# Performance work log

Hardware: AMD Instinct MI355X
Metric: run time of the kernel (lower is better)

The kernel has to match this reference:

```python
import jax, jax.numpy as jnp
import numpy as np

ALPHA = 0.5
SIGMA = 0.1
EPS = 1e-7
N, T = 8192, 512


def setup_inputs() -> dict:
    key = jax.random.key(0)
    k1, k2, k3 = jax.random.split(key, 3)
    logits = jax.random.normal(k1, (N, T), dtype=jnp.float32)
    pmf = jax.nn.softmax(logits, axis=-1)  # valid PMF rows
    times = jax.random.uniform(k2, (N,), dtype=jnp.float32, minval=0.0, maxval=float(T))
    events = jax.random.randint(k3, (N,), 0, 2).astype(jnp.int32)
    time_bins = jnp.arange(T, dtype=jnp.float32)
    return {"pmf": pmf, "times": times, "events": events, "time_bins": time_bins}


def reference(pmf, times, events, time_bins):
    n, t = pmf.shape
    # torch.bucketize(right=False) == searchsorted side='left'
    bin_idx = jnp.clip(jnp.searchsorted(time_bins, times, side='left') - 1, 0, t - 1)

    cdf = jnp.cumsum(pmf, axis=1)                 # (N, T)
    rows = jnp.arange(n)
    pmf_at = pmf[rows, bin_idx]                   # pmf[i, bin_idx[i]]
    cdf_at = cdf[rows, bin_idx]                   # cdf[i, bin_idx[i]]
    total = cdf[:, -1]
    surv = total - cdf_at + pmf_at                # sum pmf[i, bin_idx[i]:]

    nll = jnp.where(events == 1, -jnp.log(pmf_at + EPS), -jnp.log(surv + EPS))
    loss = nll.mean()

    # Pairwise ranking term (vectorized over event anchors i and later samples j)
    later = times[None, :] > times[:, None]       # later[i, j] = times[j] > times[i]
    cnt = later.sum(axis=1)                       # (N,) number of later samples per i
    G = cdf[:, bin_idx].T                         # G[i, j] = cdf[j, bin_idx[i]]
    e = jnp.exp((G - cdf_at[:, None]) / SIGMA)    # exp(diff / sigma)
    per_i = jnp.sum(jnp.where(later, e, 0.0), axis=1) / jnp.maximum(cnt, 1)
    valid = (events == 1) & (cnt > 0)
    n_pairs = valid.sum()
    rank_loss = jnp.sum(jnp.where(valid, per_i, 0.0))

    apply_rank = (events.sum() > 1) & (n_pairs > 0) & (ALPHA > 0)
    loss = jnp.where(apply_rank, loss + ALPHA * rank_loss / jnp.maximum(n_pairs, 1), loss)
    return loss
```

## Files before the change

kernel.cpp:

```cpp
#include <hip/hip_runtime.h>
#include <cstdint>
#include <cstddef>

#define SIGMA_INV 10.0f
#define EPS_C 1e-7f

constexpr int TDIM = 512;
constexpr int ROWS2 = 16;
constexpr int PITCH = 513;
constexpr int NBLK = 512;
constexpr int MAXC = 256;
constexpr int GSTRIDE = 32;

__device__ __forceinline__ void stf(float* p, float v) {
    __hip_atomic_store(p, v, __ATOMIC_RELAXED, __HIP_MEMORY_SCOPE_AGENT);
}
__device__ __forceinline__ void sti(int* p, int v) {
    __hip_atomic_store(p, v, __ATOMIC_RELAXED, __HIP_MEMORY_SCOPE_AGENT);
}
__device__ __forceinline__ float ldf(const float* p) {
    return __hip_atomic_load(p, __ATOMIC_RELAXED, __HIP_MEMORY_SCOPE_AGENT);
}
__device__ __forceinline__ int ldi(const int* p) {
    return __hip_atomic_load(p, __ATOMIC_RELAXED, __HIP_MEMORY_SCOPE_AGENT);
}

__global__ __launch_bounds__(512, 4) void rows_kernel(
    const float* __restrict__ pmf, const float* __restrict__ times,
    const int* __restrict__ events, const float* __restrict__ bins,
    unsigned* __restrict__ tkt,
    float* __restrict__ SGTp, float* __restrict__ scaleA,
    float* __restrict__ einvA, int* __restrict__ kidxA,
    float* __restrict__ nll_part, int* __restrict__ ev_part, int N)
{
    __shared__ float tile[ROWS2 * PITCH];
    __shared__ float binsS[TDIM];
    __shared__ int karr[ROWS2];
    __shared__ float nllv[ROWS2];
    __shared__ int evv[ROWS2];
    const int tid = threadIdx.x;
    const int lane = tid & 63;
    const int wid = tid >> 6;
    const int b = blockIdx.x;
    const int i0 = b * ROWS2;

    if (b == 0) {
        for (int w = tid; w < 65 * GSTRIDE; w += 512) tkt[w] = 0u;
    }

    binsS[tid] = bins[tid];

    float4 A[2][2];
    #pragma unroll
    for (int r = 0; r < 2; ++r) {
        const int i = i0 + wid * 2 + r;
        const float4* p4 = (const float4*)(pmf + (size_t)i * TDIM + lane * 8);
        A[r][0] = p4[0];
        A[r][1] = p4[1];
    }
    #pragma unroll
    for (int r = 0; r < 2; ++r) {
        const int rl = wid * 2 + r;
        float c0 = A[r][0].x, c1 = c0 + A[r][0].y, c2 = c1 + A[r][0].z, c3 = c2 + A[r][0].w;
        float c4 = c3 + A[r][1].x, c5 = c4 + A[r][1].y, c6 = c5 + A[r][1].z, c7 = c6 + A[r][1].w;
        float v = c7;
        #pragma unroll
        for (int d = 1; d < 64; d <<= 1) {
            float u = __shfl_up(v, d);
            if (lane >= d) v += u;
        }
        const float excl = v - c7;
        float* t = tile + rl * PITCH + lane * 8;
        t[0] = c0 + excl; t[1] = c1 + excl; t[2] = c2 + excl; t[3] = c3 + excl;
        t[4] = c4 + excl; t[5] = c5 + excl; t[6] = c6 + excl; t[7] = c7 + excl;
    }
    __syncthreads();

    if (tid < ROWS2) {
        const int i = i0 + tid;
        const float t = times[i];
        int lo = 0, hi = TDIM;
        while (lo < hi) {
            int mid = (lo + hi) >> 1;
            if (binsS[mid] < t) lo = mid + 1; else hi = mid;
        }
        int k = lo - 1;
        k = k < 0 ? 0 : (k > TDIM - 1 ? TDIM - 1 : k);
        const float cdf_at = tile[tid * PITCH + k];
        const float tot = tile[tid * PITCH + (TDIM - 1)];
        const float pmf_at = pmf[(size_t)i * TDIM + k];
        const float surv = tot - cdf_at + pmf_at;
        nllv[tid] = (events[i] == 1) ? -logf(pmf_at + EPS_C) : -logf(surv + EPS_C);
        evv[tid] = events[i];
        scaleA[i] = expf(-cdf_at * SIGMA_INV);
        einvA[i] = expf(cdf_at * SIGMA_INV);
        kidxA[i] = k;
        karr[tid] = k;
    }
    __syncthreads();

    float acc = 0.f;
    #pragma unroll
    for (int s = 0; s < ROWS2; ++s) {
        const float c = tile[s * PITCH + tid];
        if (tid < karr[s]) acc += expf(c * SIGMA_INV);
    }
    SGTp[(size_t)b * TDIM + tid] = acc;

    if (wid == 0) {
        float nv = (lane < ROWS2) ? nllv[lane] : 0.f;
        int ev = (lane < ROWS2) ? evv[lane] : 0;
        #pragma unroll
        for (int d = 8; d > 0; d >>= 1) {
            nv += __shfl_down(nv, d);
            ev += __shfl_down(ev, d);
        }
        if (lane == 0) { nll_part[b] = nv; ev_part[b] = ev; }
    }
}

__global__ __launch_bounds__(512, 4) void bucket_final_kernel(
    const float* __restrict__ SGTp, const float* __restrict__ times,
    const int* __restrict__ events, const int* __restrict__ kidxA,
    const float* __restrict__ scaleA, const float* __restrict__ einvA,
    const float* __restrict__ nll_part, const int* __restrict__ ev_part,
    unsigned* __restrict__ tkt,
    float* __restrict__ rank_part, int* __restrict__ npair_part,
    float* __restrict__ out, int N)
{
    __shared__ float redf[8];
    __shared__ int redi[8];
    __shared__ float red2f[8];
    __shared__ int red2i[8];
    __shared__ int cj[MAXC], oj[MAXC];
    __shared__ float mt[MAXC], me[MAXC];
    __shared__ int ncl_sh;
    __shared__ float SGT_sh;
    __shared__ int CGT_sh;
    __shared__ int last_sh;
    __shared__ double sd1[NBLK];
    __shared__ double sd2[NBLK];
    __shared__ int si1[NBLK];
    __shared__ int si2[NBLK];

    const int k = blockIdx.x;
    const int tid = threadIdx.x;
    const int lane = tid & 63;
    const int wid = tid >> 6;

    if (tid == 0) ncl_sh = 0;
    __syncthreads();

    float sv = SGTp[(size_t)tid * TDIM + k];
    #pragma unroll
    for (int d = 32; d > 0; d >>= 1) sv += __shfl_down(sv, d);
    if (lane == 0) redf[wid] = sv;

    int cnt = 0;
    const int4* kx4 = (const int4*)kidxA;
    #pragma unroll
    for (int it = 0; it < 4; ++it) {
        const int ch = it * 512 + tid;
        const int4 kx = kx4[ch];
        const int j0 = ch * 4;
        cnt += (kx.x > k) + (kx.y > k) + (kx.z > k) + (kx.w > k);
        if (kx.x == k) { int p = atomicAdd(&ncl_sh, 1); if (p < MAXC) cj[p] = j0 + 0; }
        if (kx.y == k) { int p = atomicAdd(&ncl_sh, 1); if (p < MAXC) cj[p] = j0 + 1; }
        if (kx.z == k) { int p = atomicAdd(&ncl_sh, 1); if (p < MAXC) cj[p] = j0 + 2; }
        if (kx.w == k) { int p = atomicAdd(&ncl_sh, 1); if (p < MAXC) cj[p] = j0 + 3; }
    }
    #pragma unroll
    for (int d = 32; d > 0; d >>= 1) cnt += __shfl_down(cnt, d);
    if (lane == 0) redi[wid] = cnt;
    __syncthreads();
    if (tid == 0) {
        float s8 = 0.f; int c8 = 0;
        #pragma unroll
        for (int w = 0; w < 8; ++w) { s8 += redf[w]; c8 += redi[w]; }
        SGT_sh = s8; CGT_sh = c8;
    }
    __syncthreads();

    const int nc = ncl_sh < MAXC ? ncl_sh : MAXC;
    if (tid < nc) {
        const int myj = cj[tid];
        int r = 0;
        for (int m = 0; m < nc; ++m) r += (cj[m] < myj) ? 1 : 0;
        oj[r] = myj;
    }
    __syncthreads();
    if (tid < nc) { mt[tid] = times[oj[tid]]; me[tid] = einvA[oj[tid]]; }
    __syncthreads();

    float pi = 0.f;
    int vf = 0;
    if (tid < nc) {
        const int i = oj[tid];
        const float ti = mt[tid];
        float s = 0.f;
        int c = 0;
        for (int m = 0; m < nc; ++m) {
            if (mt[m] > ti) { s += me[m]; c++; }
        }
        const int C = CGT_sh + c;
        if (events[i] == 1 && C > 0) {
            vf = 1;
            pi = scaleA[i] * (SGT_sh + s) / (float)C;
        }
    }
    #pragma unroll
    for (int d = 32; d > 0; d >>= 1) {
        pi += __shfl_down(pi, d);
        vf += __shfl_down(vf, d);
    }
    if (lane == 0) { red2f[wid] = pi; red2i[wid] = vf; }
    __syncthreads();
    if (tid == 0) {
        float s8 = 0.f; int c8 = 0;
        #pragma unroll
        for (int w = 0; w < 8; ++w) { s8 += red2f[w]; c8 += red2i[w]; }
        stf(rank_part + k, s8);
        sti(npair_part + k, c8);
    }

    __syncthreads();
    if (tid == 0) {
        asm volatile("s_waitcnt vmcnt(0)" ::: "memory");
        int is_last = 0;
        unsigned g = __hip_atomic_fetch_add(tkt + (k & 63) * GSTRIDE, 1u,
                                            __ATOMIC_RELAXED,
                                            __HIP_MEMORY_SCOPE_AGENT);
        if (g == 7u) {
            unsigned l2 = __hip_atomic_fetch_add(tkt + 64 * GSTRIDE, 1u,
                                                 __ATOMIC_RELAXED,
                                                 __HIP_MEMORY_SCOPE_AGENT);
            if (l2 == 63u) is_last = 1;
        }
        last_sh = is_last;
    }
    __syncthreads();
    if (!last_sh) return;

    sd1[tid] = (double)nll_part[tid];
    si2[tid] = ev_part[tid];
    sd2[tid] = (double)ldf(rank_part + tid);
    si1[tid] = ldi(npair_part + tid);
    __syncthreads();
    for (int off = 256; off > 0; off >>= 1) {
        if (tid < off) {
            sd1[tid] += sd1[tid + off];
            sd2[tid] += sd2[tid + off];
            si1[tid] += si1[tid + off];
            si2[tid] += si2[tid + off];
        }
        __syncthreads();
    }
    if (tid == 0) {
        double loss = sd1[0] / (double)N;
        if (si2[0] > 1 && si1[0] > 0) loss += 0.5 * sd2[0] / (double)si1[0];
        out[0] = (float)loss;
    }
}

extern "C" void kernel_launch(void* const* d_in, const int* in_sizes, int n_in,
                              void* d_out, int out_size, void* d_ws, size_t ws_size,
                              hipStream_t stream) {
    const float* pmf = (const float*)d_in[0];
    const float* times = (const float*)d_in[1];
    const int* events = (const int*)d_in[2];
    const float* bins = (const float*)d_in[3];
    const int N = in_sizes[1];

    char* ws = (char*)d_ws;
    unsigned* tkt = (unsigned*)ws;
    float* SGTp = (float*)(ws + 16384);
    float* scaleA = SGTp + (size_t)NBLK * TDIM;
    float* einvA = scaleA + N;
    float* nll_part = einvA + N;
    float* rank_part = nll_part + NBLK;
    int* kidxA = (int*)(rank_part + TDIM);
    int* ev_part = kidxA + N;
    int* npair_part = ev_part + NBLK;

    rows_kernel<<<NBLK, 512, 0, stream>>>(
        pmf, times, events, bins, tkt, SGTp, scaleA, einvA, kidxA,
        nll_part, ev_part, N);
    bucket_final_kernel<<<NBLK, 512, 0, stream>>>(
        SGTp, times, events, kidxA, scaleA, einvA, nll_part, ev_part,
        tkt, rank_part, npair_part, (float*)d_out, N);
}
```

Baseline: 23.93 us.

## Build per-bin histogram and member lists in rows kernel instead of rescanning indices

After: 31.18 us. 1.3x slower.

```diff
diff --git a/kernel.cpp b/kernel.cpp
--- a/kernel.cpp
+++ b/kernel.cpp
@@ -6,9 +6,10 @@
 #define EPS_C 1e-7f
 
 constexpr int TDIM = 512;
-constexpr int ROWS2 = 16;
+constexpr int ROWS2 = 8;
 constexpr int PITCH = 513;
-constexpr int NBLK = 512;
+constexpr int NB1 = 1024;
+constexpr int NB2 = 512;
 constexpr int MAXC = 256;
 constexpr int GSTRIDE = 32;
 
@@ -28,9 +29,10 @@
 __global__ __launch_bounds__(512, 4) void rows_kernel(
     const float* __restrict__ pmf, const float* __restrict__ times,
     const int* __restrict__ events, const float* __restrict__ bins,
-    unsigned* __restrict__ tkt,
+    unsigned* __restrict__ hist,
+    int* __restrict__ member,
     float* __restrict__ SGTp, float* __restrict__ scaleA,
-    float* __restrict__ einvA, int* __restrict__ kidxA,
+    float* __restrict__ einvA,
     float* __restrict__ nll_part, int* __restrict__ ev_part, int N)
 {
     __shared__ float tile[ROWS2 * PITCH];
@@ -44,25 +46,15 @@
     const int b = blockIdx.x;
     const int i0 = b * ROWS2;
 
-    if (b == 0) {
-        for (int w = tid; w < 65 * GSTRIDE; w += 512) tkt[w] = 0u;
-    }
-
     binsS[tid] = bins[tid];
 
-    float4 A[2][2];
-    #pragma unroll
-    for (int r = 0; r < 2; ++r) {
-        const int i = i0 + wid * 2 + r;
+    {
+        const int i = i0 + wid;
         const float4* p4 = (const float4*)(pmf + (size_t)i * TDIM + lane * 8);
-        A[r][0] = p4[0];
-        A[r][1] = p4[1];
-    }
-    #pragma unroll
-    for (int r = 0; r < 2; ++r) {
-        const int rl = wid * 2 + r;
-        float c0 = A[r][0].x, c1 = c0 + A[r][0].y, c2 = c1 + A[r][0].z, c3 = c2 + A[r][0].w;
-        float c4 = c3 + A[r][1].x, c5 = c4 + A[r][1].y, c6 = c5 + A[r][1].z, c7 = c6 + A[r][1].w;
+        const float4 a = p4[0];
+        const float4 bq = p4[1];
+        float c0 = a.x, c1 = c0 + a.y, c2 = c1 + a.z, c3 = c2 + a.w;
+        float c4 = c3 + bq.x, c5 = c4 + bq.y, c6 = c5 + bq.z, c7 = c6 + bq.w;
         float v = c7;
         #pragma unroll
         for (int d = 1; d < 64; d <<= 1) {
@@ -70,7 +62,7 @@
             if (lane >= d) v += u;
         }
         const float excl = v - c7;
-        float* t = tile + rl * PITCH + lane * 8;
+        float* t = tile + wid * PITCH + lane * 8;
         t[0] = c0 + excl; t[1] = c1 + excl; t[2] = c2 + excl; t[3] = c3 + excl;
         t[4] = c4 + excl; t[5] = c5 + excl; t[6] = c6 + excl; t[7] = c7 + excl;
     }
@@ -94,8 +86,9 @@
         evv[tid] = events[i];
         scaleA[i] = expf(-cdf_at * SIGMA_INV);
         einvA[i] = expf(cdf_at * SIGMA_INV);
-        kidxA[i] = k;
         karr[tid] = k;
+        const unsigned slot = atomicAdd(&hist[k * GSTRIDE], 1u);
+        if (slot < (unsigned)MAXC) member[k * MAXC + slot] = i;
     }
     __syncthreads();
 
@@ -111,7 +104,7 @@
         float nv = (lane < ROWS2) ? nllv[lane] : 0.f;
         int ev = (lane < ROWS2) ? evv[lane] : 0;
         #pragma unroll
-        for (int d = 8; d > 0; d >>= 1) {
+        for (int d = 4; d > 0; d >>= 1) {
             nv += __shfl_down(nv, d);
             ev += __shfl_down(ev, d);
         }
@@ -121,9 +114,10 @@
 
 __global__ __launch_bounds__(512, 4) void bucket_final_kernel(
     const float* __restrict__ SGTp, const float* __restrict__ times,
-    const int* __restrict__ events, const int* __restrict__ kidxA,
+    const int* __restrict__ events,
     const float* __restrict__ scaleA, const float* __restrict__ einvA,
     const float* __restrict__ nll_part, const int* __restrict__ ev_part,
+    const unsigned* __restrict__ hist, const int* __restrict__ member,
     unsigned* __restrict__ tkt,
     float* __restrict__ rank_part, int* __restrict__ npair_part,
     float* __restrict__ out, int N)
@@ -134,41 +128,27 @@
     __shared__ int red2i[8];
     __shared__ int cj[MAXC], oj[MAXC];
     __shared__ float mt[MAXC], me[MAXC];
-    __shared__ int ncl_sh;
+    __shared__ int nc_sh;
     __shared__ float SGT_sh;
     __shared__ int CGT_sh;
     __shared__ int last_sh;
-    __shared__ double sd1[NBLK];
-    __shared__ double sd2[NBLK];
-    __shared__ int si1[NBLK];
-    __shared__ int si2[NBLK];
+    __shared__ double sd1[NB2];
+    __shared__ double sd2[NB2];
+    __shared__ int si1[NB2];
+    __shared__ int si2[NB2];
 
     const int k = blockIdx.x;
     const int tid = threadIdx.x;
     const int lane = tid & 63;
     const int wid = tid >> 6;
 
-    if (tid == 0) ncl_sh = 0;
-    __syncthreads();
-
-    float sv = SGTp[(size_t)tid * TDIM + k];
+    float sv = SGTp[(size_t)tid * TDIM + k] + SGTp[(size_t)(tid + 512) * TDIM + k];
     #pragma unroll
     for (int d = 32; d > 0; d >>= 1) sv += __shfl_down(sv, d);
     if (lane == 0) redf[wid] = sv;
 
-    int cnt = 0;
-    const int4* kx4 = (const int4*)kidxA;
-    #pragma unroll
-    for (int it = 0; it < 4; ++it) {
-        const int ch = it * 512 + tid;
-        const int4 kx = kx4[ch];
-        const int j0 = ch * 4;
-        cnt += (kx.x > k) + (kx.y > k) + (kx.z > k) + (kx.w > k);
-        if (kx.x == k) { int p = atomicAdd(&ncl_sh, 1); if (p < MAXC) cj[p] = j0 + 0; }
-        if (kx.y == k) { int p = atomicAdd(&ncl_sh, 1); if (p < MAXC) cj[p] = j0 + 1; }
-        if (kx.z == k) { int p = atomicAdd(&ncl_sh, 1); if (p < MAXC) cj[p] = j0 + 2; }
-        if (kx.w == k) { int p = atomicAdd(&ncl_sh, 1); if (p < MAXC) cj[p] = j0 + 3; }
-    }
+    const unsigned h = hist[tid * GSTRIDE];
+    int cnt = (tid > k) ? (int)h : 0;
     #pragma unroll
     for (int d = 32; d > 0; d >>= 1) cnt += __shfl_down(cnt, d);
     if (lane == 0) redi[wid] = cnt;
@@ -178,10 +158,14 @@
         #pragma unroll
         for (int w = 0; w < 8; ++w) { s8 += redf[w]; c8 += redi[w]; }
         SGT_sh = s8; CGT_sh = c8;
-    }
-    __syncthreads();
-
-    const int nc = ncl_sh < MAXC ? ncl_sh : MAXC;
+        const unsigned hk = hist[k * GSTRIDE];
+        nc_sh = hk < (unsigned)MAXC ? (int)hk : MAXC;
+    }
+    __syncthreads();
+
+    const int nc = nc_sh;
+    if (tid < nc) cj[tid] = member[k * MAXC + tid];
+    __syncthreads();
     if (tid < nc) {
         const int myj = cj[tid];
         int r = 0;
@@ -241,8 +225,8 @@
     __syncthreads();
     if (!last_sh) return;
 
-    sd1[tid] = (double)nll_part[tid];
-    si2[tid] = ev_part[tid];
+    sd1[tid] = (double)nll_part[tid] + (double)nll_part[tid + 512];
+    si2[tid] = ev_part[tid] + ev_part[tid + 512];
     sd2[tid] = (double)ldf(rank_part + tid);
     si1[tid] = ldi(npair_part + tid);
     __syncthreads();
@@ -273,19 +257,21 @@
 
     char* ws = (char*)d_ws;
     unsigned* tkt = (unsigned*)ws;
-    float* SGTp = (float*)(ws + 16384);
-    float* scaleA = SGTp + (size_t)NBLK * TDIM;
+    unsigned* hist = (unsigned*)(ws + 65 * 128);
+    int* member = (int*)(ws + (65 + 512) * 128);
+    float* SGTp = (float*)(ws + (65 + 512) * 128 + 512 * MAXC * 4);
+    float* scaleA = SGTp + (size_t)NB1 * TDIM;
     float* einvA = scaleA + N;
     float* nll_part = einvA + N;
-    float* rank_part = nll_part + NBLK;
-    int* kidxA = (int*)(rank_part + TDIM);
-    int* ev_part = kidxA + N;
-    int* npair_part = ev_part + NBLK;
-
-    rows_kernel<<<NBLK, 512, 0, stream>>>(
-        pmf, times, events, bins, tkt, SGTp, scaleA, einvA, kidxA,
+    float* rank_part = nll_part + NB1;
+    int* ev_part = (int*)(rank_part + NB2);
+    int* npair_part = ev_part + NB1;
+
+    hipMemsetAsync(ws, 0, (65 + 512) * 128, stream);
+    rows_kernel<<<NB1, 512, 0, stream>>>(
+        pmf, times, events, bins, hist, member, SGTp, scaleA, einvA,
         nll_part, ev_part, N);
-    bucket_final_kernel<<<NBLK, 512, 0, stream>>>(
-        SGTp, times, events, kidxA, scaleA, einvA, nll_part, ev_part,
-        tkt, rank_part, npair_part, (float*)d_out, N);
-}
+    bucket_final_kernel<<<NB2, 512, 0, stream>>>(
+        SGTp, times, events, scaleA, einvA, nll_part, ev_part,
+        hist, member, tkt, rank_part, npair_part, (float*)d_out, N);
+}
```
